# Optimization experiments

Measured on AMD Instinct MI355X. Metric: run time of the kernel, lower is better.

## Reference

```python
import jax, jax.numpy as jnp
import numpy as np

TOPK = 9
NUM_CLASSES = 80
NUM_ANCHORS_LIST = [6400, 1600, 400]  # strides 8/16/32 on 640x640
EPS = 1e-9


def bbox_center(b):
    return (b[..., :2] + b[..., 2:]) * 0.5


def pairwise_iou(b1, b2):
    # b1: (B,n,4), b2: (B or 1, L, 4) -> (B,n,L)
    lt = jnp.maximum(b1[:, :, None, :2], b2[:, None, :, :2])
    rb = jnp.minimum(b1[:, :, None, 2:], b2[:, None, :, 2:])
    wh = jnp.clip(rb - lt, 0.0)
    inter = wh[..., 0] * wh[..., 1]
    a1 = (b1[..., 2] - b1[..., 0]) * (b1[..., 3] - b1[..., 1])
    a2 = (b2[..., 2] - b2[..., 0]) * (b2[..., 3] - b2[..., 1])
    union = a1[:, :, None] + a2[:, None, :] - inter + EPS
    return inter / union


def atss_forward(anchor_bboxes, gt_labels, gt_bboxes, pad_gt_mask, pred_bboxes, bg_index):
    B, n = gt_bboxes.shape[:2]
    L = anchor_bboxes.shape[0]
    dt = gt_bboxes.dtype

    ious = pairwise_iou(gt_bboxes, anchor_bboxes[None])              # (B,n,L)
    gt_c = bbox_center(gt_bboxes)                                    # (B,n,2)
    a_c = bbox_center(anchor_bboxes)                                 # (L,2)
    dists = jnp.linalg.norm(gt_c[:, :, None] - a_c[None, None], axis=-1)  # (B,n,L)

    pad_bool = pad_gt_mask[..., 0] > 0                               # (B,n)
    bi = jnp.arange(B)[:, None, None]
    gi = jnp.arange(n)[None, :, None]
    is_in_topk_parts, topk_idx_parts = [], []
    start = 0
    for nl in NUM_ANCHORS_LIST:  # fixed small set of pyramid levels
        d = jax.lax.dynamic_slice_in_dim(dists, start, nl, axis=-1)
        _, idx = jax.lax.top_k(-d, TOPK)                             # k smallest distances
        topk_idx_parts.append(idx + start)
        idx0 = jnp.where(pad_bool[..., None], idx, 0)
        # scatter-count instead of materializing (B,n,TOPK,nl) one-hot
        cnt = jnp.zeros((B, n, nl), dt).at[bi, gi, idx0].add(1.0)
        is_in_topk_parts.append(jnp.where(cnt > 1, 0.0, cnt))
        start += nl
    is_in_topk = jnp.concatenate(is_in_topk_parts, -1)               # (B,n,L)
    topk_idxs = jnp.concatenate(topk_idx_parts, -1)                  # (B,n,3*TOPK)

    iou_cand = ious * is_in_topk
    thr_samp = jnp.take_along_axis(iou_cand, topk_idxs, axis=-1)     # (B,n,27)
    thr = thr_samp.mean(-1, keepdims=True) + jnp.std(thr_samp, axis=-1, keepdims=True, ddof=1)
    is_in_topk = jnp.where(iou_cand > thr, is_in_topk, 0.0)

    # anchor centers strictly inside gt boxes
    lt = a_c[None, None] - gt_bboxes[:, :, None, :2]
    rb = gt_bboxes[:, :, None, 2:] - a_c[None, None]
    is_in_gts = (jnp.minimum(lt, rb).min(-1) > EPS).astype(dt)       # (B,n,L)

    mask_positive = is_in_topk * is_in_gts * pad_gt_mask             # (B,n,L)
    mps = mask_positive.sum(1)                                       # (B,L)

    # anchors matched to multiple gts -> keep highest-iou gt (no-op if none)
    multi = mps[:, None, :] > 1
    max_idx = jnp.argmax(ious, axis=1)                               # (B,L)
    is_max_iou = (jnp.arange(n)[None, :, None] == max_idx[:, None, :]).astype(dt)
    mask_positive = jnp.where(multi, is_max_iou, mask_positive)
    mps = mask_positive.sum(1)

    agi = jnp.argmax(mask_positive, axis=1)                          # (B,L)
    labels = jnp.take_along_axis(gt_labels[..., 0], agi, axis=1)
    labels = jnp.where(mps > 0, labels, bg_index).astype(jnp.int32)
    bboxes = jnp.take_along_axis(gt_bboxes, agi[..., None], axis=1)  # (B,L,4)

    scores = jax.nn.one_hot(labels, NUM_CLASSES + 1, dtype=jnp.float32)
    keep = np.array([i for i in range(NUM_CLASSES + 1) if i != bg_index])
    scores = scores[..., keep]                                       # (B,L,C)

    ious_pred = pairwise_iou(gt_bboxes, pred_bboxes) * mask_positive
    scores = scores * ious_pred.max(1)[..., None]
    return labels, bboxes, scores


def setup_inputs() -> dict:
    key = jax.random.key(0)
    ks = jax.random.split(key, 6)
    B, n = 32, 128
    anchors = []
    for fs, stride in [(80, 8), (40, 16), (20, 32)]:
        xs = (jnp.arange(fs, dtype=jnp.float32) + 0.5) * stride
        cy, cx = jnp.meshgrid(xs, xs, indexing='ij')
        c = jnp.stack([cx.ravel(), cy.ravel()], -1)
        half = 2.5 * stride
        anchors.append(jnp.concatenate([c - half, c + half], -1))
    anchor_bboxes = jnp.concatenate(anchors, 0)                      # (8400,4)
    L = anchor_bboxes.shape[0]
    cxy = jax.random.uniform(ks[0], (B, n, 2), minval=0.0, maxval=640.0)
    wh = jax.random.uniform(ks[1], (B, n, 2), minval=10.0, maxval=300.0)
    gt_bboxes = jnp.concatenate([cxy - wh / 2, cxy + wh / 2], -1)
    gt_labels = jax.random.randint(ks[2], (B, n, 1), 0, 80).astype(jnp.int32)
    nvalid = jax.random.randint(ks[3], (B, 1), 16, n + 1)
    pad_gt_mask = (jnp.arange(n)[None] < nvalid).astype(jnp.float32)[..., None]
    a_c = bbox_center(anchor_bboxes)
    pc = a_c[None] + 8.0 * jax.random.normal(ks[4], (B, L, 2))
    pwh = jax.random.uniform(ks[5], (B, L, 2), minval=20.0, maxval=200.0)
    pred_bboxes = jnp.concatenate([pc - pwh / 2, pc + pwh / 2], -1)
    return {"anchor_bboxes": anchor_bboxes, "gt_labels": gt_labels,
            "gt_bboxes": gt_bboxes, "pad_gt_mask": pad_gt_mask,
            "pred_bboxes": pred_bboxes, "bg_index": 80}


def reference(anchor_bboxes, gt_labels, gt_bboxes, pad_gt_mask, pred_bboxes, bg_index):
    return atss_forward(anchor_bboxes, gt_labels, gt_bboxes, pad_gt_mask, pred_bboxes, bg_index)
```

## Files before the change

kernel.cpp:

```cpp
#include <hip/hip_runtime.h>
#include <cstdint>

#define NB   32
#define NGT  128
#define NL   8400
#define TK   9
#define NC   80
#define FEPS 1e-9f

__device__ __forceinline__ float iou_box(float ax0, float ay0, float ax1, float ay1,
                                         float bx0, float by0, float bx1, float by1) {
#pragma clang fp contract(off)
    float lx = fmaxf(ax0, bx0), ly = fmaxf(ay0, by0);
    float rx = fminf(ax1, bx1), ry = fminf(ay1, by1);
    float w = fmaxf(rx - lx, 0.f), h = fmaxf(ry - ly, 0.f);
    float inter = w * h;
    float a1 = (ax1 - ax0) * (ay1 - ay0);
    float a2 = (bx1 - bx0) * (by1 - by0);
    float uni = a1 + a2 - inter + FEPS;
    return inter / uni;
}

__device__ __forceinline__ unsigned long long shfl_xor_u64(unsigned long long v, int off) {
    unsigned int lo = (unsigned int)v, hi = (unsigned int)(v >> 32);
    lo = __shfl_xor(lo, off, 64);
    hi = __shfl_xor(hi, off, 64);
    return ((unsigned long long)hi << 32) | lo;
}

__device__ __forceinline__ void anchor_box(int a, float& x0, float& y0, float& x1, float& y1) {
    int fs, rem; float s;
    if (a < 6400)      { fs = 80; s = 8.f;  rem = a; }
    else if (a < 8000) { fs = 40; s = 16.f; rem = a - 6400; }
    else               { fs = 20; s = 32.f; rem = a - 8000; }
    int iy = rem / fs, ix = rem - iy * fs;
    float cx = ((float)ix + 0.5f) * s, cy = ((float)iy + 0.5f) * s, h = 2.5f * s;
    x0 = cx - h; y0 = cy - h; x1 = cx + h; y1 = cy + h;
}

__global__ void __launch_bounds__(256)
atss_topk_kernel(const float* __restrict__ gtb, const float* __restrict__ padm,
                 unsigned int* __restrict__ cmask) {
#pragma clang fp contract(off)
    const int lane = threadIdx.x & 63;
    const int p = blockIdx.x * 4 + (threadIdx.x >> 6);
    const int b = p >> 7, g = p & 127;
    if (padm[b * NGT + g] <= 0.f) return;

    const float* gp = gtb + (size_t)(b * NGT + g) * 4;
    const float gx0 = gp[0], gy0 = gp[1], gx1 = gp[2], gy1 = gp[3];
    const float gcx = (gx0 + gx1) * 0.5f, gcy = (gy0 + gy1) * 0.5f;

    const int   fs_[3]   = {80, 40, 20};
    const float st_[3]   = {8.f, 16.f, 32.f};
    const int   base_[3] = {0, 6400, 8000};

    int myA = -1;
    int cnt = 0;
    for (int lv = 0; lv < 3; ++lv) {
        const int fs = fs_[lv]; const float s = st_[lv]; const int base = base_[lv];
        const int fx = (int)floorf(gcx / s - 0.5f);
        const int fy = (int)floorf(gcy / s - 0.5f);
        const int lox = min(max(fx - 4, 0), fs - 10);
        const int loy = min(max(fy - 4, 0), fs - 10);

        unsigned long long k0 = ~0ULL, k1 = ~0ULL;
        {
            const int k = lane;
            const int iy = loy + k / 10, ix = lox + k - (k / 10) * 10;
            const float ax = ((float)ix + 0.5f) * s, ay = ((float)iy + 0.5f) * s;
            const float dx = gcx - ax, dy = gcy - ay;
            const float d = sqrtf(dx * dx + dy * dy);
            const int gidx = base + iy * fs + ix;
            k0 = ((unsigned long long)__float_as_uint(d) << 32) | (unsigned int)gidx;
        }
        if (lane + 64 < 100) {
            const int k = lane + 64;
            const int iy = loy + k / 10, ix = lox + k - (k / 10) * 10;
            const float ax = ((float)ix + 0.5f) * s, ay = ((float)iy + 0.5f) * s;
            const float dx = gcx - ax, dy = gcy - ay;
            const float d = sqrtf(dx * dx + dy * dy);
            const int gidx = base + iy * fs + ix;
            k1 = ((unsigned long long)__float_as_uint(d) << 32) | (unsigned int)gidx;
        }
        if (k1 < k0) { unsigned long long t = k0; k0 = k1; k1 = t; }

        int ptr = 0;
        for (int r = 0; r < TK; ++r) {
            const unsigned long long h = (ptr == 0) ? k0 : (ptr == 1 ? k1 : ~0ULL);
            unsigned long long m = h;
            for (int off = 32; off >= 1; off >>= 1) {
                const unsigned long long o = shfl_xor_u64(m, off);
                if (o < m) m = o;
            }
            if (m == h) ptr++;
            if (lane == cnt) myA = (int)(unsigned int)(m & 0xffffffffu);
            cnt++;
        }
    }

    float myiou = 0.f, acx = 0.f, acy = 0.f;
    const bool sel = (myA >= 0);
    if (sel) {
        float ax0, ay0, ax1, ay1;
        anchor_box(myA, ax0, ay0, ax1, ay1);
        myiou = iou_box(gx0, gy0, gx1, gy1, ax0, ay0, ax1, ay1);
        acx = (ax0 + ax1) * 0.5f;
        acy = (ay0 + ay1) * 0.5f;
    }
    float ssum = sel ? myiou : 0.f;
    for (int off = 32; off >= 1; off >>= 1) ssum += __shfl_xor(ssum, off, 64);
    const float mean = ssum / 27.f;
    float d2 = sel ? (myiou - mean) * (myiou - mean) : 0.f;
    for (int off = 32; off >= 1; off >>= 1) d2 += __shfl_xor(d2, off, 64);
    const float thr = mean + sqrtf(d2 / 26.f);

    if (sel && myiou > thr) {
        const float l = acx - gx0, t = acy - gy0, r = gx1 - acx, bo = gy1 - acy;
        const float mn = fminf(fminf(l, t), fminf(r, bo));
        if (mn > FEPS) {
            atomicOr(&cmask[(size_t)(b * NL + myA) * 4 + (g >> 5)], 1u << (g & 31));
        }
    }
}

__global__ void __launch_bounds__(256)
atss_assign_kernel(const int* __restrict__ gtl, const float* __restrict__ gtb,
                   const float* __restrict__ pred, const int* __restrict__ bgp,
                   const uint4* __restrict__ cmask, float* __restrict__ out) {
#pragma clang fp contract(off)
    __shared__ float4 sgt[NGT];
    __shared__ int    slbl[NGT];
    __shared__ int    s_lab[256];
    __shared__ float  s_iou[256];

    const int tid = threadIdx.x;
    const int b = blockIdx.y;
    const int a0 = blockIdx.x * 256;
    const int a = a0 + tid;

    if (tid < NGT) {
        sgt[tid]  = ((const float4*)gtb)[b * NGT + tid];
        slbl[tid] = gtl[b * NGT + tid];
    }
    __syncthreads();

    int lbl = 0, pos = 0;
    float ioup = 0.f;
    if (a < NL) {
        const int t = b * NL + a;
        const uint4 m = cmask[t];
        const int mps = __popc(m.x) + __popc(m.y) + __popc(m.z) + __popc(m.w);
        int agi = 0;
        if (mps > 1) {
            float ax0, ay0, ax1, ay1;
            anchor_box(a, ax0, ay0, ax1, ay1);
            float best = -1.f;
            for (int gg = 0; gg < NGT; ++gg) {
                const float4 gb = sgt[gg];
                const float v = iou_box(gb.x, gb.y, gb.z, gb.w, ax0, ay0, ax1, ay1);
                if (v > best) { best = v; agi = gg; }
            }
            pos = 1;
        } else if (mps == 1) {
            if (m.x)      agi = __ffs(m.x) - 1;
            else if (m.y) agi = 32 + __ffs(m.y) - 1;
            else if (m.z) agi = 64 + __ffs(m.z) - 1;
            else          agi = 96 + __ffs(m.w) - 1;
            pos = 1;
        }
        const int bgi = *bgp;
        lbl = pos ? slbl[agi] : bgi;
        out[t] = (float)lbl;

        const float4 gb = sgt[agi];
        ((float4*)(out + (size_t)NB * NL))[t] = gb;

        if (pos) {
            const float4 pb = ((const float4*)pred)[t];
            ioup = iou_box(gb.x, gb.y, gb.z, gb.w, pb.x, pb.y, pb.z, pb.w);
        }
    }
    s_lab[tid] = pos ? lbl : -1;
    s_iou[tid] = ioup;
    __syncthreads();

    const int nA = min(256, NL - a0);
    float* osb = out + (size_t)NB * NL * 5 + ((size_t)b * NL + a0) * NC;
    const int total = nA * NC;
    for (int e = tid; e < total; e += 256) {
        const int ai = e / NC;
        const int c = e - ai * NC;
        osb[e] = (c == s_lab[ai]) ? s_iou[ai] : 0.f;
    }
}

extern "C" void kernel_launch(void* const* d_in, const int* in_sizes, int n_in,
                              void* d_out, int out_size, void* d_ws, size_t ws_size,
                              hipStream_t stream) {
    const int*   gtl  = (const int*)d_in[1];
    const float* gtb  = (const float*)d_in[2];
    const float* padm = (const float*)d_in[3];
    const float* pred = (const float*)d_in[4];
    const int*   bgp  = (const int*)d_in[5];

    unsigned int* cmask = (unsigned int*)d_ws;
    (void)hipMemsetAsync(cmask, 0, (size_t)NB * NL * 4 * sizeof(unsigned int), stream);

    atss_topk_kernel<<<NB * NGT / 4, 256, 0, stream>>>(gtb, padm, cmask);

    dim3 grid((NL + 255) / 256, NB);
    atss_assign_kernel<<<grid, 256, 0, stream>>>(gtl, gtb, pred, bgp,
                                                 (const uint4*)cmask, (float*)d_out);
}
```

Baseline: 148.0 us.

## Replace global candidate bitmask with compact per-GT candidate list and per-thread top-k

The top-k kernel now gives each thread one (GT, level) pair and keeps a register insertion-sorted top-9 instead of wave-wide shuffle reductions. It writes a compact list of 27 candidate anchor ids per GT instead of atomically OR-ing a global bitmask, which removes the memset of the mask buffer. The assign kernel builds the per-anchor mask in shared memory by scanning all 128x27 candidates of the batch, and it vectorises the one-hot score output to float4 stores. In exchange, every assign block redundantly reads the whole candidate list for its batch and performs shared atomics.

Result: slower. 151.5 us (+2.4%).

```diff
diff --git a/kernel.cpp b/kernel.cpp
--- a/kernel.cpp
+++ b/kernel.cpp
@@ -7,6 +7,8 @@
 #define TK   9
 #define NC   80
 #define FEPS 1e-9f
+
+typedef unsigned long long u64;
 
 __device__ __forceinline__ float iou_box(float ax0, float ay0, float ax1, float ay1,
                                          float bx0, float by0, float bx1, float by1) {
@@ -21,13 +23,6 @@
     return inter / uni;
 }
 
-__device__ __forceinline__ unsigned long long shfl_xor_u64(unsigned long long v, int off) {
-    unsigned int lo = (unsigned int)v, hi = (unsigned int)(v >> 32);
-    lo = __shfl_xor(lo, off, 64);
-    hi = __shfl_xor(hi, off, 64);
-    return ((unsigned long long)hi << 32) | lo;
-}
-
 __device__ __forceinline__ void anchor_box(int a, float& x0, float& y0, float& x1, float& y1) {
     int fs, rem; float s;
     if (a < 6400)      { fs = 80; s = 8.f;  rem = a; }
@@ -38,88 +33,101 @@
     x0 = cx - h; y0 = cy - h; x1 = cx + h; y1 = cy + h;
 }
 
-__global__ void __launch_bounds__(256)
+__global__ void __launch_bounds__(192)
 atss_topk_kernel(const float* __restrict__ gtb, const float* __restrict__ padm,
-                 unsigned int* __restrict__ cmask) {
+                 int* __restrict__ cand) {
 #pragma clang fp contract(off)
-    const int lane = threadIdx.x & 63;
-    const int p = blockIdx.x * 4 + (threadIdx.x >> 6);
-    const int b = p >> 7, g = p & 127;
-    if (padm[b * NGT + g] <= 0.f) return;
-
-    const float* gp = gtb + (size_t)(b * NGT + g) * 4;
-    const float gx0 = gp[0], gy0 = gp[1], gx1 = gp[2], gy1 = gp[3];
+    __shared__ float siou[64][27];
+    __shared__ int   sidx[64][27];
+
+    const int tid = threadIdx.x;
+    const int gl  = tid & 63;
+    const int lv  = tid >> 6;
+    const int p   = blockIdx.x * 64 + gl;
+
+    const float4 gb = ((const float4*)gtb)[p];
+    const float gx0 = gb.x, gy0 = gb.y, gx1 = gb.z, gy1 = gb.w;
     const float gcx = (gx0 + gx1) * 0.5f, gcy = (gy0 + gy1) * 0.5f;
 
-    const int   fs_[3]   = {80, 40, 20};
-    const float st_[3]   = {8.f, 16.f, 32.f};
-    const int   base_[3] = {0, 6400, 8000};
-
-    int myA = -1;
-    int cnt = 0;
-    for (int lv = 0; lv < 3; ++lv) {
-        const int fs = fs_[lv]; const float s = st_[lv]; const int base = base_[lv];
+    {
+        const int   fs   = (lv == 0) ? 80 : (lv == 1 ? 40 : 20);
+        const float s    = (lv == 0) ? 8.f : (lv == 1 ? 16.f : 32.f);
+        const int   base = (lv == 0) ? 0 : (lv == 1 ? 6400 : 8000);
+
         const int fx = (int)floorf(gcx / s - 0.5f);
         const int fy = (int)floorf(gcy / s - 0.5f);
         const int lox = min(max(fx - 4, 0), fs - 10);
         const int loy = min(max(fy - 4, 0), fs - 10);
 
-        unsigned long long k0 = ~0ULL, k1 = ~0ULL;
-        {
-            const int k = lane;
-            const int iy = loy + k / 10, ix = lox + k - (k / 10) * 10;
-            const float ax = ((float)ix + 0.5f) * s, ay = ((float)iy + 0.5f) * s;
-            const float dx = gcx - ax, dy = gcy - ay;
-            const float d = sqrtf(dx * dx + dy * dy);
-            const int gidx = base + iy * fs + ix;
-            k0 = ((unsigned long long)__float_as_uint(d) << 32) | (unsigned int)gidx;
-        }
-        if (lane + 64 < 100) {
-            const int k = lane + 64;
-            const int iy = loy + k / 10, ix = lox + k - (k / 10) * 10;
-            const float ax = ((float)ix + 0.5f) * s, ay = ((float)iy + 0.5f) * s;
-            const float dx = gcx - ax, dy = gcy - ay;
-            const float d = sqrtf(dx * dx + dy * dy);
-            const int gidx = base + iy * fs + ix;
-            k1 = ((unsigned long long)__float_as_uint(d) << 32) | (unsigned int)gidx;
-        }
-        if (k1 < k0) { unsigned long long t = k0; k0 = k1; k1 = t; }
-
-        int ptr = 0;
-        for (int r = 0; r < TK; ++r) {
-            const unsigned long long h = (ptr == 0) ? k0 : (ptr == 1 ? k1 : ~0ULL);
-            unsigned long long m = h;
-            for (int off = 32; off >= 1; off >>= 1) {
-                const unsigned long long o = shfl_xor_u64(m, off);
-                if (o < m) m = o;
+        u64 sk[TK];
+#pragma unroll
+        for (int j = 0; j < TK; ++j) sk[j] = ~0ULL;
+
+        for (int r = 0; r < 10; ++r) {
+            const int iy = loy + r;
+            const float ay = ((float)iy + 0.5f) * s;
+            const float dy = gcy - ay;
+            const float dy2 = dy * dy;
+            const int rowbase = base + iy * fs + lox;
+#pragma unroll
+            for (int c = 0; c < 10; ++c) {
+                const float ax = ((float)(lox + c) + 0.5f) * s;
+                const float dx = gcx - ax;
+                const float d = sqrtf(dx * dx + dy2);
+                u64 nk = ((u64)__float_as_uint(d) << 32) | (unsigned int)(rowbase + c);
+#pragma unroll
+                for (int j = 0; j < TK; ++j) {
+                    const u64 sj = sk[j];
+                    const u64 mn = (nk < sj) ? nk : sj;
+                    nk = (nk < sj) ? sj : nk;
+                    sk[j] = mn;
+                }
             }
-            if (m == h) ptr++;
-            if (lane == cnt) myA = (int)(unsigned int)(m & 0xffffffffu);
-            cnt++;
-        }
-    }
-
-    float myiou = 0.f, acx = 0.f, acy = 0.f;
-    const bool sel = (myA >= 0);
-    if (sel) {
-        float ax0, ay0, ax1, ay1;
-        anchor_box(myA, ax0, ay0, ax1, ay1);
-        myiou = iou_box(gx0, gy0, gx1, gy1, ax0, ay0, ax1, ay1);
-        acx = (ax0 + ax1) * 0.5f;
-        acy = (ay0 + ay1) * 0.5f;
-    }
-    float ssum = sel ? myiou : 0.f;
-    for (int off = 32; off >= 1; off >>= 1) ssum += __shfl_xor(ssum, off, 64);
-    const float mean = ssum / 27.f;
-    float d2 = sel ? (myiou - mean) * (myiou - mean) : 0.f;
-    for (int off = 32; off >= 1; off >>= 1) d2 += __shfl_xor(d2, off, 64);
-    const float thr = mean + sqrtf(d2 / 26.f);
-
-    if (sel && myiou > thr) {
-        const float l = acx - gx0, t = acy - gy0, r = gx1 - acx, bo = gy1 - acy;
-        const float mn = fminf(fminf(l, t), fminf(r, bo));
-        if (mn > FEPS) {
-            atomicOr(&cmask[(size_t)(b * NL + myA) * 4 + (g >> 5)], 1u << (g & 31));
+        }
+
+#pragma unroll
+        for (int j = 0; j < TK; ++j) {
+            const int id = (int)(unsigned int)(sk[j] & 0xffffffffu);
+            float ax0, ay0, ax1, ay1;
+            anchor_box(id, ax0, ay0, ax1, ay1);
+            siou[gl][lv * TK + j] = iou_box(gx0, gy0, gx1, gy1, ax0, ay0, ax1, ay1);
+            sidx[gl][lv * TK + j] = id;
+        }
+    }
+    __syncthreads();
+
+    if (tid < 64) {
+        int* cp = cand + (size_t)p * 27;
+        if (padm[p] <= 0.f) {
+#pragma unroll
+            for (int k = 0; k < 27; ++k) cp[k] = -1;
+            return;
+        }
+        float sum = 0.f;
+#pragma unroll
+        for (int k = 0; k < 27; ++k) sum += siou[gl][k];
+        const float mean = sum / 27.f;
+        float d2 = 0.f;
+#pragma unroll
+        for (int k = 0; k < 27; ++k) {
+            const float e = siou[gl][k] - mean;
+            d2 += e * e;
+        }
+        const float thr = mean + sqrtf(d2 / 26.f);
+
+#pragma unroll
+        for (int k = 0; k < 27; ++k) {
+            const int id = sidx[gl][k];
+            int keep = -1;
+            if (siou[gl][k] > thr) {
+                float ax0, ay0, ax1, ay1;
+                anchor_box(id, ax0, ay0, ax1, ay1);
+                const float acx = (ax0 + ax1) * 0.5f, acy = (ay0 + ay1) * 0.5f;
+                const float l = acx - gx0, t = acy - gy0, r = gx1 - acx, bo = gy1 - acy;
+                const float mn = fminf(fminf(l, t), fminf(r, bo));
+                if (mn > FEPS) keep = id;
+            }
+            cp[k] = keep;
         }
     }
 }
@@ -127,8 +135,9 @@
 __global__ void __launch_bounds__(256)
 atss_assign_kernel(const int* __restrict__ gtl, const float* __restrict__ gtb,
                    const float* __restrict__ pred, const int* __restrict__ bgp,
-                   const uint4* __restrict__ cmask, float* __restrict__ out) {
+                   const int* __restrict__ cand, float* __restrict__ out) {
 #pragma clang fp contract(off)
+    __shared__ unsigned int smask[256][4];
     __shared__ float4 sgt[NGT];
     __shared__ int    slbl[NGT];
     __shared__ int    s_lab[256];
@@ -137,61 +146,81 @@
     const int tid = threadIdx.x;
     const int b = blockIdx.y;
     const int a0 = blockIdx.x * 256;
-    const int a = a0 + tid;
-
+    const int nA = min(256, NL - a0);
+
+    smask[tid][0] = 0; smask[tid][1] = 0; smask[tid][2] = 0; smask[tid][3] = 0;
     if (tid < NGT) {
         sgt[tid]  = ((const float4*)gtb)[b * NGT + tid];
         slbl[tid] = gtl[b * NGT + tid];
     }
     __syncthreads();
 
+    const int* cb = cand + (size_t)b * NGT * 27;
+    for (int f = tid; f < NGT * 27; f += 256) {
+        const int id = cb[f];
+        const int la = id - a0;
+        if (la >= 0 && la < nA) {
+            const int g = f / 27;
+            atomicOr(&smask[la][g >> 5], 1u << (g & 31));
+        }
+    }
+    __syncthreads();
+
     int lbl = 0, pos = 0;
     float ioup = 0.f;
+    const int a = a0 + tid;
     if (a < NL) {
         const int t = b * NL + a;
-        const uint4 m = cmask[t];
-        const int mps = __popc(m.x) + __popc(m.y) + __popc(m.z) + __popc(m.w);
+        const unsigned int m0 = smask[tid][0], m1 = smask[tid][1];
+        const unsigned int m2 = smask[tid][2], m3 = smask[tid][3];
+        const int mps = __popc(m0) + __popc(m1) + __popc(m2) + __popc(m3);
         int agi = 0;
         if (mps > 1) {
             float ax0, ay0, ax1, ay1;
             anchor_box(a, ax0, ay0, ax1, ay1);
             float best = -1.f;
             for (int gg = 0; gg < NGT; ++gg) {
-                const float4 gb = sgt[gg];
-                const float v = iou_box(gb.x, gb.y, gb.z, gb.w, ax0, ay0, ax1, ay1);
+                const float4 q = sgt[gg];
+                const float v = iou_box(q.x, q.y, q.z, q.w, ax0, ay0, ax1, ay1);
                 if (v > best) { best = v; agi = gg; }
             }
             pos = 1;
         } else if (mps == 1) {
-            if (m.x)      agi = __ffs(m.x) - 1;
-            else if (m.y) agi = 32 + __ffs(m.y) - 1;
-            else if (m.z) agi = 64 + __ffs(m.z) - 1;
-            else          agi = 96 + __ffs(m.w) - 1;
+            if (m0)      agi = __ffs(m0) - 1;
+            else if (m1) agi = 32 + __ffs(m1) - 1;
+            else if (m2) agi = 64 + __ffs(m2) - 1;
+            else         agi = 96 + __ffs(m3) - 1;
             pos = 1;
         }
         const int bgi = *bgp;
         lbl = pos ? slbl[agi] : bgi;
         out[t] = (float)lbl;
 
-        const float4 gb = sgt[agi];
-        ((float4*)(out + (size_t)NB * NL))[t] = gb;
+        const float4 q = sgt[agi];
+        ((float4*)(out + (size_t)NB * NL))[t] = q;
 
         if (pos) {
             const float4 pb = ((const float4*)pred)[t];
-            ioup = iou_box(gb.x, gb.y, gb.z, gb.w, pb.x, pb.y, pb.z, pb.w);
+            ioup = iou_box(q.x, q.y, q.z, q.w, pb.x, pb.y, pb.z, pb.w);
         }
     }
     s_lab[tid] = pos ? lbl : -1;
     s_iou[tid] = ioup;
     __syncthreads();
 
-    const int nA = min(256, NL - a0);
-    float* osb = out + (size_t)NB * NL * 5 + ((size_t)b * NL + a0) * NC;
-    const int total = nA * NC;
-    for (int e = tid; e < total; e += 256) {
-        const int ai = e / NC;
-        const int c = e - ai * NC;
-        osb[e] = (c == s_lab[ai]) ? s_iou[ai] : 0.f;
+    float4* osb = (float4*)(out + (size_t)NB * NL * 5 + ((size_t)b * NL + a0) * NC);
+    const int total4 = nA * (NC / 4);
+    for (int e = tid; e < total4; e += 256) {
+        const int ai = e / (NC / 4);
+        const int c0 = (e - ai * (NC / 4)) * 4;
+        const int lb = s_lab[ai];
+        const float v = s_iou[ai];
+        float4 o;
+        o.x = (c0     == lb) ? v : 0.f;
+        o.y = (c0 + 1 == lb) ? v : 0.f;
+        o.z = (c0 + 2 == lb) ? v : 0.f;
+        o.w = (c0 + 3 == lb) ? v : 0.f;
+        osb[e] = o;
     }
 }
 
@@ -204,12 +233,10 @@
     const float* pred = (const float*)d_in[4];
     const int*   bgp  = (const int*)d_in[5];
 
-    unsigned int* cmask = (unsigned int*)d_ws;
-    (void)hipMemsetAsync(cmask, 0, (size_t)NB * NL * 4 * sizeof(unsigned int), stream);
-
-    atss_topk_kernel<<<NB * NGT / 4, 256, 0, stream>>>(gtb, padm, cmask);
+    int* cand = (int*)d_ws;
+
+    atss_topk_kernel<<<NB * NGT / 64, 192, 0, stream>>>(gtb, padm, cand);
 
     dim3 grid((NL + 255) / 256, NB);
-    atss_assign_kernel<<<grid, 256, 0, stream>>>(gtl, gtb, pred, bgp,
-                                                 (const uint4*)cmask, (float*)d_out);
-}
+    atss_assign_kernel<<<grid, 256, 0, stream>>>(gtl, gtb, pred, bgp, cand, (float*)d_out);
+}
```
